# Kernel tuning notes

Hardware: AMD Instinct MI355X
Metric: run time of the kernel (lower is better)

## Reference

```python
import jax, jax.numpy as jnp
import numpy as np

B, C, H, W = 8, 10, 128, 128  # batch, hidden_dim, spatial
EPS = 1e-5


def conv1x1(x, w, b=None):
    # x: [b, i, h, w], w: [o, i] -> [b, o, h, w]
    y = jnp.einsum('oi,bihw->bohw', w, x)
    if b is not None:
        y = y + b[None, :, None, None]
    return y


def bn(x, gamma, beta):
    # training-mode batchnorm over (N, H, W), as InPlaceABNSync(activation='none')
    m = x.mean(axis=(0, 2, 3), keepdims=True)
    v = x.var(axis=(0, 2, 3), keepdims=True)
    xn = (x - m) * jax.lax.rsqrt(v + EPS)
    return xn * gamma[None, :, None, None] + beta[None, :, None, None]


def conv_gru(x, h, wg, bg, wc):
    # ConvGRU with 1x1 kernels: gates conv -> 2 channels (reset, update)
    gates = conv1x1(jnp.concatenate([x, h], axis=1), wg, bg)  # [b,2,h,w]
    reset = jax.nn.sigmoid(gates[:, 0:1])
    update = jax.nn.sigmoid(gates[:, 1:2])
    cand = jnp.tanh(conv1x1(jnp.concatenate([x, reset * h], axis=1), wc))
    return (1.0 - update) * h + update * cand


def setup_inputs() -> dict:
    key = jax.random.key(0)
    ks = jax.random.split(key, 16)
    rn = lambda k, shape, s=1.0: jax.random.normal(k, shape, dtype=jnp.float32) * s
    inp = {
        'f0': rn(ks[0], (B, C, H, W)),
        'f1': rn(ks[1], (B, C, H, W)),
        'h0': rn(ks[2], (B, C, H, W)),
        'h1': rn(ks[3], (B, C, H, W)),
        'h2': rn(ks[4], (B, C, H, W)),
        # Composition.comp_att: Conv2d(2C -> 1, bias=True) + Sigmoid
        'W_att': rn(ks[5], (1, 2 * C), 0.1),
        'b_att': jnp.zeros((1,), jnp.float32),
        # Composition.relation: Conv(2C->2C, no bias) BN ReLU Conv(2C->C, no bias) BN ReLU
        'W_r1': rn(ks[6], (2 * C, 2 * C), 0.1),
        'g_r1': jnp.ones((2 * C,), jnp.float32),
        'be_r1': jnp.zeros((2 * C,), jnp.float32),
        'W_r2': rn(ks[7], (C, 2 * C), 0.1),
        'g_r2': jnp.ones((C,), jnp.float32),
        'be_r2': jnp.zeros((C,), jnp.float32),
        # ConvGRU update[0]: gates Conv(2C->2, bias) ; candidate Conv(2C->C, no bias)
        'Wg0': rn(ks[8], (2, 2 * C), 0.1),
        'bg0': jnp.zeros((2,), jnp.float32),
        'Wc0': rn(ks[9], (C, 2 * C), 0.1),
        # ConvGRU update[1]
        'Wg1': rn(ks[10], (2, 2 * C), 0.1),
        'bg1': jnp.zeros((2,), jnp.float32),
        'Wc1': rn(ks[11], (C, 2 * C), 0.1),
    }
    return inp


def reference(f0, f1, h0, h1, h2,
              W_att, b_att, W_r1, g_r1, be_r1, W_r2, g_r2, be_r2,
              Wg0, bg0, Wc0, Wg1, bg1, Wc1):
    # node 0: update[0](h_node_list[0], f_node_list[0])
    node0 = conv_gru(h0, f0, Wg0, bg0, Wc0)
    # Composition over children h1, h2
    comp_att = jax.nn.sigmoid(conv1x1(jnp.concatenate([h1, h2], axis=1), W_att, b_att))  # [b,1,h,w]
    x = jnp.concatenate([f1, (h1 + h2) * comp_att], axis=1)  # [b,2C,h,w]
    x = jax.nn.relu(bn(conv1x1(x, W_r1), g_r1, be_r1))
    comp_full = jax.nn.relu(bn(conv1x1(x, W_r2), g_r2, be_r2))  # [b,C,h,w]
    # node 1: update[1](comp_full, f_node_list[1])
    node1 = conv_gru(comp_full, f1, Wg1, bg1, Wc1)
    return node0, node1, comp_att
```

## Files before the change

kernel.cpp:

```cpp
#include <hip/hip_runtime.h>
#include <math.h>

#define HW     16384
#define CDIM   10
#define NPIX   131072
#define NPLANE 1310720
#define BN_N   131072.0f
#define EPS_BN 1e-5f

__device__ __forceinline__ float sigf(float x) { return 1.0f / (1.0f + __expf(-x)); }
__device__ __forceinline__ float tanh_fast(float x) {
    x = fminf(fmaxf(x, -15.0f), 15.0f);
    float e = __expf(2.0f * x);
    return (e - 1.0f) / (e + 1.0f);
}
__device__ __forceinline__ float wred(float v) {
#pragma unroll
    for (int o = 32; o; o >>= 1) v += __shfl_down(v, o, 64);
    return v;
}

__global__ __launch_bounds__(256) void kernA(
    const float* __restrict__ f0, const float* __restrict__ f1,
    const float* __restrict__ h0, const float* __restrict__ h1, const float* __restrict__ h2,
    const float* __restrict__ W_att, const float* __restrict__ b_att,
    const float* __restrict__ W_r1,
    const float* __restrict__ Wg0, const float* __restrict__ bg0, const float* __restrict__ Wc0,
    float* __restrict__ node0, float* __restrict__ att_out, float* __restrict__ stats1)
{
    __shared__ float sW1[400], sWatt[20], sWg[40], sWc[200];
    __shared__ float sPart[4 * 40];
    const int tid = threadIdx.x;
    for (int i = tid; i < 400; i += 256) sW1[i] = W_r1[i];
    for (int i = tid; i < 200; i += 256) sWc[i] = Wc0[i];
    if (tid < 20) sWatt[tid] = W_att[tid];
    if (tid < 40) sWg[tid] = Wg0[tid];
    __syncthreads();
    const float batt = b_att[0], bg_r = bg0[0], bg_u = bg0[1];
    const int p = blockIdx.x * 256 + tid;
    const int b = p >> 14, s = p & 16383;
    const int base = b * (CDIM * HW) + s;
    const int wave = tid >> 6, lane = tid & 63;

    float vh1[10], vh2[10], vf1[10];
#pragma unroll
    for (int c = 0; c < 10; c++) {
        vh1[c] = h1[base + c * HW];
        vh2[c] = h2[base + c * HW];
        vf1[c] = f1[base + c * HW];
    }
    float z = batt;
#pragma unroll
    for (int c = 0; c < 10; c++) z += sWatt[c] * vh1[c] + sWatt[10 + c] * vh2[c];
    const float att = sigf(z);
    att_out[p] = att;

    float x[20];
#pragma unroll
    for (int c = 0; c < 10; c++) { x[c] = vf1[c]; x[10 + c] = (vh1[c] + vh2[c]) * att; }
#pragma unroll
    for (int o = 0; o < 20; o++) {
        float acc = 0.0f;
#pragma unroll
        for (int i = 0; i < 20; i++) acc = fmaf(sW1[o * 20 + i], x[i], acc);
        float q = acc * acc;
        float rs = wred(acc);
        float rq = wred(q);
        if (lane == 0) { sPart[wave * 40 + o] = rs; sPart[wave * 40 + 20 + o] = rq; }
    }
    __syncthreads();
    if (tid < 40) {
        float t = sPart[tid] + sPart[40 + tid] + sPart[80 + tid] + sPart[120 + tid];
        atomicAdd(&stats1[tid], t);
    }

    float vf0[10], vh0[10];
#pragma unroll
    for (int c = 0; c < 10; c++) { vf0[c] = f0[base + c * HW]; vh0[c] = h0[base + c * HW]; }
    float g0 = bg_r, g1 = bg_u;
#pragma unroll
    for (int i = 0; i < 10; i++) {
        g0 += sWg[i] * vh0[i] + sWg[10 + i] * vf0[i];
        g1 += sWg[20 + i] * vh0[i] + sWg[30 + i] * vf0[i];
    }
    const float r = sigf(g0), u = sigf(g1);
#pragma unroll
    for (int o = 0; o < 10; o++) {
        float acc = 0.0f;
#pragma unroll
        for (int i = 0; i < 10; i++) acc = fmaf(sWc[o * 20 + i], vh0[i], acc);
#pragma unroll
        for (int i = 0; i < 10; i++) acc = fmaf(sWc[o * 20 + 10 + i], r * vf0[i], acc);
        node0[base + o * HW] = (1.0f - u) * vf0[o] + u * tanh_fast(acc);
    }
}

__global__ __launch_bounds__(256) void kernC(
    const float* __restrict__ f1, const float* __restrict__ h1, const float* __restrict__ h2,
    const float* __restrict__ att_in,
    const float* __restrict__ W_r1, const float* __restrict__ g_r1, const float* __restrict__ be_r1,
    const float* __restrict__ W_r2,
    const float* __restrict__ stats1, float* __restrict__ y2out, float* __restrict__ stats2)
{
    __shared__ float sW1[400], sW2[200], sA[20], sB[20];
    __shared__ float sPart[4 * 20];
    const int tid = threadIdx.x;
    for (int i = tid; i < 400; i += 256) sW1[i] = W_r1[i];
    for (int i = tid; i < 200; i += 256) sW2[i] = W_r2[i];
    if (tid < 20) {
        float sm = stats1[tid], sq = stats1[20 + tid];
        float mean = sm * (1.0f / BN_N);
        float var = sq * (1.0f / BN_N) - mean * mean;
        float a = g_r1[tid] * rsqrtf(var + EPS_BN);
        sA[tid] = a;
        sB[tid] = be_r1[tid] - mean * a;
    }
    __syncthreads();
    const int p = blockIdx.x * 256 + tid;
    const int b = p >> 14, s = p & 16383;
    const int base = b * (CDIM * HW) + s;
    const int wave = tid >> 6, lane = tid & 63;

    float vh1[10], vh2[10], vf1[10];
#pragma unroll
    for (int c = 0; c < 10; c++) {
        vh1[c] = h1[base + c * HW];
        vh2[c] = h2[base + c * HW];
        vf1[c] = f1[base + c * HW];
    }
    const float att = att_in[p];
    float x[20];
#pragma unroll
    for (int c = 0; c < 10; c++) { x[c] = vf1[c]; x[10 + c] = (vh1[c] + vh2[c]) * att; }
    float x2[20];
#pragma unroll
    for (int o = 0; o < 20; o++) {
        float acc = 0.0f;
#pragma unroll
        for (int i = 0; i < 20; i++) acc = fmaf(sW1[o * 20 + i], x[i], acc);
        x2[o] = fmaxf(fmaf(sA[o], acc, sB[o]), 0.0f);
    }
    const int base2 = b * (10 * HW) + s;
#pragma unroll
    for (int o = 0; o < 10; o++) {
        float acc = 0.0f;
#pragma unroll
        for (int i = 0; i < 20; i++) acc = fmaf(sW2[o * 20 + i], x2[i], acc);
        y2out[base2 + o * HW] = acc;
        float q = acc * acc;
        float rs = wred(acc);
        float rq = wred(q);
        if (lane == 0) { sPart[wave * 20 + o] = rs; sPart[wave * 20 + 10 + o] = rq; }
    }
    __syncthreads();
    if (tid < 20) {
        float t = sPart[tid] + sPart[20 + tid] + sPart[40 + tid] + sPart[60 + tid];
        atomicAdd(&stats2[tid], t);
    }
}

__global__ __launch_bounds__(256) void kernE(
    const float* __restrict__ f1, const float* __restrict__ y2in,
    const float* __restrict__ stats2,
    const float* __restrict__ g_r2, const float* __restrict__ be_r2,
    const float* __restrict__ Wg1, const float* __restrict__ bg1, const float* __restrict__ Wc1,
    float* __restrict__ node1)
{
    __shared__ float sWg[40], sWc[200], sA[10], sB[10];
    const int tid = threadIdx.x;
    for (int i = tid; i < 200; i += 256) sWc[i] = Wc1[i];
    if (tid < 40) sWg[tid] = Wg1[tid];
    if (tid < 10) {
        float sm = stats2[tid], sq = stats2[10 + tid];
        float mean = sm * (1.0f / BN_N);
        float var = sq * (1.0f / BN_N) - mean * mean;
        float a = g_r2[tid] * rsqrtf(var + EPS_BN);
        sA[tid] = a;
        sB[tid] = be_r2[tid] - mean * a;
    }
    __syncthreads();
    const float bg_r = bg1[0], bg_u = bg1[1];
    const int p = blockIdx.x * 256 + tid;
    const int b = p >> 14, s = p & 16383;
    const int base = b * (CDIM * HW) + s;

    float comp[10], vf1[10];
#pragma unroll
    for (int c = 0; c < 10; c++) {
        vf1[c] = f1[base + c * HW];
        comp[c] = fmaxf(fmaf(sA[c], y2in[base + c * HW], sB[c]), 0.0f);
    }
    float g0 = bg_r, g1 = bg_u;
#pragma unroll
    for (int i = 0; i < 10; i++) {
        g0 += sWg[i] * comp[i] + sWg[10 + i] * vf1[i];
        g1 += sWg[20 + i] * comp[i] + sWg[30 + i] * vf1[i];
    }
    const float r = sigf(g0), u = sigf(g1);
#pragma unroll
    for (int o = 0; o < 10; o++) {
        float acc = 0.0f;
#pragma unroll
        for (int i = 0; i < 10; i++) acc = fmaf(sWc[o * 20 + i], comp[i], acc);
#pragma unroll
        for (int i = 0; i < 10; i++) acc = fmaf(sWc[o * 20 + 10 + i], r * vf1[i], acc);
        node1[base + o * HW] = (1.0f - u) * vf1[o] + u * tanh_fast(acc);
    }
}

extern "C" void kernel_launch(void* const* d_in, const int* in_sizes, int n_in,
                              void* d_out, int out_size, void* d_ws, size_t ws_size,
                              hipStream_t stream) {
    const float* f0    = (const float*)d_in[0];
    const float* f1    = (const float*)d_in[1];
    const float* h0    = (const float*)d_in[2];
    const float* h1    = (const float*)d_in[3];
    const float* h2    = (const float*)d_in[4];
    const float* W_att = (const float*)d_in[5];
    const float* b_att = (const float*)d_in[6];
    const float* W_r1  = (const float*)d_in[7];
    const float* g_r1  = (const float*)d_in[8];
    const float* be_r1 = (const float*)d_in[9];
    const float* W_r2  = (const float*)d_in[10];
    const float* g_r2  = (const float*)d_in[11];
    const float* be_r2 = (const float*)d_in[12];
    const float* Wg0   = (const float*)d_in[13];
    const float* bg0   = (const float*)d_in[14];
    const float* Wc0   = (const float*)d_in[15];
    const float* Wg1   = (const float*)d_in[16];
    const float* bg1   = (const float*)d_in[17];
    const float* Wc1   = (const float*)d_in[18];

    float* out   = (float*)d_out;
    float* node0 = out;
    float* node1 = out + NPLANE;
    float* attO  = out + 2 * NPLANE;

    float* y2     = (float*)d_ws;
    float* stats1 = y2 + (size_t)10 * NPIX;
    float* stats2 = stats1 + 40;

    hipMemsetAsync(stats1, 0, 64 * sizeof(float), stream);

    dim3 grid(NPIX / 256), blk(256);
    kernA<<<grid, blk, 0, stream>>>(f0, f1, h0, h1, h2, W_att, b_att, W_r1,
                                    Wg0, bg0, Wc0, node0, attO, stats1);
    kernC<<<grid, blk, 0, stream>>>(f1, h1, h2, attO, W_r1, g_r1, be_r1, W_r2,
                                    stats1, y2, stats2);
    kernE<<<grid, blk, 0, stream>>>(f1, y2, stats2, g_r2, be_r2, Wg1, bg1, Wc1,
                                    node1);
}
```

Before: 148.0 us.

## Use scalar weight loads, DPP wave reductions, recompute attention, reorder GRU work

Drops the shared-memory weight staging and its barrier in all three kernels, so weights are read directly from global memory as uniform scalar loads. Replaces the shuffle-based wave reduction with a DPP row-shift/broadcast sequence whose total lands in lane 63. kernC now recomputes the attention sigmoid from h1/h2 instead of reading the att buffer written by kernA. In kernA all five inputs are loaded up front and the node0 GRU runs before the BN statistics. The costs are higher register pressure from holding 50 loaded values and a little extra arithmetic in kernC.

New measurement: 148.8 us. Within noise of the previous version (+0.6%).

```diff
diff --git a/kernel.cpp b/kernel.cpp
--- a/kernel.cpp
+++ b/kernel.cpp
@@ -14,10 +14,20 @@
     float e = __expf(2.0f * x);
     return (e - 1.0f) / (e + 1.0f);
 }
-__device__ __forceinline__ float wred(float v) {
-#pragma unroll
-    for (int o = 32; o; o >>= 1) v += __shfl_down(v, o, 64);
-    return v;
+
+template<int CTRL>
+__device__ __forceinline__ float dpp_add(float x) {
+    int t = __builtin_amdgcn_update_dpp(0, __float_as_int(x), CTRL, 0xF, 0xF, true);
+    return x + __int_as_float(t);
+}
+__device__ __forceinline__ float wred63(float x) {
+    x = dpp_add<0x111>(x);
+    x = dpp_add<0x112>(x);
+    x = dpp_add<0x114>(x);
+    x = dpp_add<0x118>(x);
+    x = dpp_add<0x142>(x);
+    x = dpp_add<0x143>(x);
+    return x;
 }
 
 __global__ __launch_bounds__(256) void kernA(
@@ -28,30 +38,43 @@
     const float* __restrict__ Wg0, const float* __restrict__ bg0, const float* __restrict__ Wc0,
     float* __restrict__ node0, float* __restrict__ att_out, float* __restrict__ stats1)
 {
-    __shared__ float sW1[400], sWatt[20], sWg[40], sWc[200];
     __shared__ float sPart[4 * 40];
     const int tid = threadIdx.x;
-    for (int i = tid; i < 400; i += 256) sW1[i] = W_r1[i];
-    for (int i = tid; i < 200; i += 256) sWc[i] = Wc0[i];
-    if (tid < 20) sWatt[tid] = W_att[tid];
-    if (tid < 40) sWg[tid] = Wg0[tid];
-    __syncthreads();
-    const float batt = b_att[0], bg_r = bg0[0], bg_u = bg0[1];
     const int p = blockIdx.x * 256 + tid;
     const int b = p >> 14, s = p & 16383;
     const int base = b * (CDIM * HW) + s;
     const int wave = tid >> 6, lane = tid & 63;
 
-    float vh1[10], vh2[10], vf1[10];
+    float vh1[10], vh2[10], vf1[10], vf0[10], vh0[10];
 #pragma unroll
     for (int c = 0; c < 10; c++) {
         vh1[c] = h1[base + c * HW];
         vh2[c] = h2[base + c * HW];
         vf1[c] = f1[base + c * HW];
-    }
-    float z = batt;
-#pragma unroll
-    for (int c = 0; c < 10; c++) z += sWatt[c] * vh1[c] + sWatt[10 + c] * vh2[c];
+        vf0[c] = f0[base + c * HW];
+        vh0[c] = h0[base + c * HW];
+    }
+
+    float g0 = bg0[0], g1 = bg0[1];
+#pragma unroll
+    for (int i = 0; i < 10; i++) {
+        g0 = fmaf(Wg0[i],      vh0[i], fmaf(Wg0[10 + i], vf0[i], g0));
+        g1 = fmaf(Wg0[20 + i], vh0[i], fmaf(Wg0[30 + i], vf0[i], g1));
+    }
+    const float r = sigf(g0), u = sigf(g1);
+#pragma unroll
+    for (int o = 0; o < 10; o++) {
+        float acc = 0.0f;
+#pragma unroll
+        for (int i = 0; i < 10; i++) acc = fmaf(Wc0[o * 20 + i], vh0[i], acc);
+#pragma unroll
+        for (int i = 0; i < 10; i++) acc = fmaf(Wc0[o * 20 + 10 + i], r * vf0[i], acc);
+        node0[base + o * HW] = (1.0f - u) * vf0[o] + u * tanh_fast(acc);
+    }
+
+    float z = b_att[0];
+#pragma unroll
+    for (int c = 0; c < 10; c++) z = fmaf(W_att[c], vh1[c], fmaf(W_att[10 + c], vh2[c], z));
     const float att = sigf(z);
     att_out[p] = att;
 
@@ -62,65 +85,42 @@
     for (int o = 0; o < 20; o++) {
         float acc = 0.0f;
 #pragma unroll
-        for (int i = 0; i < 20; i++) acc = fmaf(sW1[o * 20 + i], x[i], acc);
-        float q = acc * acc;
-        float rs = wred(acc);
-        float rq = wred(q);
-        if (lane == 0) { sPart[wave * 40 + o] = rs; sPart[wave * 40 + 20 + o] = rq; }
+        for (int i = 0; i < 20; i++) acc = fmaf(W_r1[o * 20 + i], x[i], acc);
+        float rs = wred63(acc);
+        float rq = wred63(acc * acc);
+        if (lane == 63) { sPart[wave * 40 + o] = rs; sPart[wave * 40 + 20 + o] = rq; }
     }
     __syncthreads();
     if (tid < 40) {
         float t = sPart[tid] + sPart[40 + tid] + sPart[80 + tid] + sPart[120 + tid];
         atomicAdd(&stats1[tid], t);
     }
-
-    float vf0[10], vh0[10];
-#pragma unroll
-    for (int c = 0; c < 10; c++) { vf0[c] = f0[base + c * HW]; vh0[c] = h0[base + c * HW]; }
-    float g0 = bg_r, g1 = bg_u;
-#pragma unroll
-    for (int i = 0; i < 10; i++) {
-        g0 += sWg[i] * vh0[i] + sWg[10 + i] * vf0[i];
-        g1 += sWg[20 + i] * vh0[i] + sWg[30 + i] * vf0[i];
-    }
-    const float r = sigf(g0), u = sigf(g1);
-#pragma unroll
-    for (int o = 0; o < 10; o++) {
-        float acc = 0.0f;
-#pragma unroll
-        for (int i = 0; i < 10; i++) acc = fmaf(sWc[o * 20 + i], vh0[i], acc);
-#pragma unroll
-        for (int i = 0; i < 10; i++) acc = fmaf(sWc[o * 20 + 10 + i], r * vf0[i], acc);
-        node0[base + o * HW] = (1.0f - u) * vf0[o] + u * tanh_fast(acc);
-    }
 }
 
 __global__ __launch_bounds__(256) void kernC(
     const float* __restrict__ f1, const float* __restrict__ h1, const float* __restrict__ h2,
-    const float* __restrict__ att_in,
+    const float* __restrict__ W_att, const float* __restrict__ b_att,
     const float* __restrict__ W_r1, const float* __restrict__ g_r1, const float* __restrict__ be_r1,
     const float* __restrict__ W_r2,
     const float* __restrict__ stats1, float* __restrict__ y2out, float* __restrict__ stats2)
 {
-    __shared__ float sW1[400], sW2[200], sA[20], sB[20];
     __shared__ float sPart[4 * 20];
     const int tid = threadIdx.x;
-    for (int i = tid; i < 400; i += 256) sW1[i] = W_r1[i];
-    for (int i = tid; i < 200; i += 256) sW2[i] = W_r2[i];
-    if (tid < 20) {
-        float sm = stats1[tid], sq = stats1[20 + tid];
-        float mean = sm * (1.0f / BN_N);
-        float var = sq * (1.0f / BN_N) - mean * mean;
-        float a = g_r1[tid] * rsqrtf(var + EPS_BN);
-        sA[tid] = a;
-        sB[tid] = be_r1[tid] - mean * a;
-    }
-    __syncthreads();
     const int p = blockIdx.x * 256 + tid;
     const int b = p >> 14, s = p & 16383;
     const int base = b * (CDIM * HW) + s;
     const int wave = tid >> 6, lane = tid & 63;
 
+    float A1[20], B1[20];
+#pragma unroll
+    for (int c = 0; c < 20; c++) {
+        float mean = stats1[c] * (1.0f / BN_N);
+        float var  = stats1[20 + c] * (1.0f / BN_N) - mean * mean;
+        float a = g_r1[c] * rsqrtf(var + EPS_BN);
+        A1[c] = a;
+        B1[c] = be_r1[c] - mean * a;
+    }
+
     float vh1[10], vh2[10], vf1[10];
 #pragma unroll
     for (int c = 0; c < 10; c++) {
@@ -128,7 +128,11 @@
         vh2[c] = h2[base + c * HW];
         vf1[c] = f1[base + c * HW];
     }
-    const float att = att_in[p];
+    float z = b_att[0];
+#pragma unroll
+    for (int c = 0; c < 10; c++) z = fmaf(W_att[c], vh1[c], fmaf(W_att[10 + c], vh2[c], z));
+    const float att = sigf(z);
+
     float x[20];
 #pragma unroll
     for (int c = 0; c < 10; c++) { x[c] = vf1[c]; x[10 + c] = (vh1[c] + vh2[c]) * att; }
@@ -137,20 +141,19 @@
     for (int o = 0; o < 20; o++) {
         float acc = 0.0f;
 #pragma unroll
-        for (int i = 0; i < 20; i++) acc = fmaf(sW1[o * 20 + i], x[i], acc);
-        x2[o] = fmaxf(fmaf(sA[o], acc, sB[o]), 0.0f);
+        for (int i = 0; i < 20; i++) acc = fmaf(W_r1[o * 20 + i], x[i], acc);
+        x2[o] = fmaxf(fmaf(A1[o], acc, B1[o]), 0.0f);
     }
     const int base2 = b * (10 * HW) + s;
 #pragma unroll
     for (int o = 0; o < 10; o++) {
         float acc = 0.0f;
 #pragma unroll
-        for (int i = 0; i < 20; i++) acc = fmaf(sW2[o * 20 + i], x2[i], acc);
+        for (int i = 0; i < 20; i++) acc = fmaf(W_r2[o * 20 + i], x2[i], acc);
         y2out[base2 + o * HW] = acc;
-        float q = acc * acc;
-        float rs = wred(acc);
-        float rq = wred(q);
-        if (lane == 0) { sPart[wave * 20 + o] = rs; sPart[wave * 20 + 10 + o] = rq; }
+        float rs = wred63(acc);
+        float rq = wred63(acc * acc);
+        if (lane == 63) { sPart[wave * 20 + o] = rs; sPart[wave * 20 + 10 + o] = rq; }
     }
     __syncthreads();
     if (tid < 20) {
@@ -166,44 +169,41 @@
     const float* __restrict__ Wg1, const float* __restrict__ bg1, const float* __restrict__ Wc1,
     float* __restrict__ node1)
 {
-    __shared__ float sWg[40], sWc[200], sA[10], sB[10];
     const int tid = threadIdx.x;
-    for (int i = tid; i < 200; i += 256) sWc[i] = Wc1[i];
-    if (tid < 40) sWg[tid] = Wg1[tid];
-    if (tid < 10) {
-        float sm = stats2[tid], sq = stats2[10 + tid];
-        float mean = sm * (1.0f / BN_N);
-        float var = sq * (1.0f / BN_N) - mean * mean;
-        float a = g_r2[tid] * rsqrtf(var + EPS_BN);
-        sA[tid] = a;
-        sB[tid] = be_r2[tid] - mean * a;
-    }
-    __syncthreads();
-    const float bg_r = bg1[0], bg_u = bg1[1];
     const int p = blockIdx.x * 256 + tid;
     const int b = p >> 14, s = p & 16383;
     const int base = b * (CDIM * HW) + s;
 
+    float A2[10], B2[10];
+#pragma unroll
+    for (int c = 0; c < 10; c++) {
+        float mean = stats2[c] * (1.0f / BN_N);
+        float var  = stats2[10 + c] * (1.0f / BN_N) - mean * mean;
+        float a = g_r2[c] * rsqrtf(var + EPS_BN);
+        A2[c] = a;
+        B2[c] = be_r2[c] - mean * a;
+    }
+
     float comp[10], vf1[10];
 #pragma unroll
     for (int c = 0; c < 10; c++) {
-        vf1[c] = f1[base + c * HW];
-        comp[c] = fmaxf(fmaf(sA[c], y2in[base + c * HW], sB[c]), 0.0f);
-    }
-    float g0 = bg_r, g1 = bg_u;
+        vf1[c]  = f1[base + c * HW];
+        comp[c] = fmaxf(fmaf(A2[c], y2in[base + c * HW], B2[c]), 0.0f);
+    }
+    float g0 = bg1[0], g1v = bg1[1];
 #pragma unroll
     for (int i = 0; i < 10; i++) {
-        g0 += sWg[i] * comp[i] + sWg[10 + i] * vf1[i];
-        g1 += sWg[20 + i] * comp[i] + sWg[30 + i] * vf1[i];
-    }
-    const float r = sigf(g0), u = sigf(g1);
+        g0  = fmaf(Wg1[i],      comp[i], fmaf(Wg1[10 + i], vf1[i], g0));
+        g1v = fmaf(Wg1[20 + i], comp[i], fmaf(Wg1[30 + i], vf1[i], g1v));
+    }
+    const float r = sigf(g0), u = sigf(g1v);
 #pragma unroll
     for (int o = 0; o < 10; o++) {
         float acc = 0.0f;
 #pragma unroll
-        for (int i = 0; i < 10; i++) acc = fmaf(sWc[o * 20 + i], comp[i], acc);
-#pragma unroll
-        for (int i = 0; i < 10; i++) acc = fmaf(sWc[o * 20 + 10 + i], r * vf1[i], acc);
+        for (int i = 0; i < 10; i++) acc = fmaf(Wc1[o * 20 + i], comp[i], acc);
+#pragma unroll
+        for (int i = 0; i < 10; i++) acc = fmaf(Wc1[o * 20 + 10 + i], r * vf1[i], acc);
         node1[base + o * HW] = (1.0f - u) * vf1[o] + u * tanh_fast(acc);
     }
 }
@@ -245,7 +245,7 @@
     dim3 grid(NPIX / 256), blk(256);
     kernA<<<grid, blk, 0, stream>>>(f0, f1, h0, h1, h2, W_att, b_att, W_r1,
                                     Wg0, bg0, Wc0, node0, attO, stats1);
-    kernC<<<grid, blk, 0, stream>>>(f1, h1, h2, attO, W_r1, g_r1, be_r1, W_r2,
+    kernC<<<grid, blk, 0, stream>>>(f1, h1, h2, W_att, b_att, W_r1, g_r1, be_r1, W_r2,
                                     stats1, y2, stats2);
     kernE<<<grid, blk, 0, stream>>>(f1, y2, stats2, g_r2, be_r2, Wg1, bg1, Wc1,
                                     node1);
```
